# Kernel tuning notes

Measured on AMD Instinct MI355X. Metric: run time of the kernel, lower is better.

## Reference

```python
import jax, jax.numpy as jnp
import numpy as np
import math

D, H, HKV = 1024, 16, 4
DH = D // H  # 64
B, T = 2, 2048


def _rope_tables(T, Dh):
    pos = jnp.arange(T, dtype=jnp.float32)
    inv_freq = 1.0 / (10000.0 ** (jnp.arange(0, Dh, 2, dtype=jnp.float32) / Dh))
    ang = pos[:, None] * inv_freq[None, :]                 # [T, Dh/2]
    ang = jnp.concatenate([ang, ang], axis=-1)             # [T, Dh]
    return jnp.cos(ang)[None, None], jnp.sin(ang)[None, None]  # [1,1,T,Dh]


def setup_inputs() -> dict:
    key = jax.random.key(0)
    kx, kq, kk, kv, ko = jax.random.split(key, 5)
    x = jax.random.normal(kx, (B, T, D), dtype=jnp.float32)
    s = 1.0 / math.sqrt(D)
    Wq = jax.random.normal(kq, (H * DH, D), dtype=jnp.float32) * s
    Wk = jax.random.normal(kk, (HKV * DH, D), dtype=jnp.float32) * s
    Wv = jax.random.normal(kv, (HKV * DH, D), dtype=jnp.float32) * s
    Wo = jax.random.normal(ko, (D, D), dtype=jnp.float32) * s
    rope_cos, rope_sin = _rope_tables(T, DH)
    # additive causal mask: 0 on/below diagonal, -1e9 above
    causal = jnp.triu(jnp.full((T, T), -1e9, dtype=jnp.float32), k=1)[None, None]
    return {"x": x, "rope_cos": rope_cos, "rope_sin": rope_sin,
            "attn_mask": causal, "Wq": Wq, "Wk": Wk, "Wv": Wv, "Wo": Wo}


def _apply_rope(t, cos, sin):
    # t: [B,h,T,Dh]; cos/sin broadcast [1,1,T,Dh]
    Dh = t.shape[-1]
    t1, t2 = t[..., :Dh // 2], t[..., Dh // 2:]
    t_rot = jnp.concatenate([-t2, t1], axis=-1)
    Tlen = t.shape[2]
    return t * cos[..., :Tlen, :] + t_rot * sin[..., :Tlen, :]


def reference(x, rope_cos, rope_sin, attn_mask, Wq, Wk, Wv, Wo):
    Bx, Tx, Dx = x.shape
    q = (x @ Wq.T).reshape(Bx, Tx, H, DH).transpose(0, 2, 1, 3)    # [B,H,T,Dh]
    k = (x @ Wk.T).reshape(Bx, Tx, HKV, DH).transpose(0, 2, 1, 3)  # [B,Hkv,T,Dh]
    v = (x @ Wv.T).reshape(Bx, Tx, HKV, DH).transpose(0, 2, 1, 3)
    q = _apply_rope(q, rope_cos, rope_sin)
    k = _apply_rope(k, rope_cos, rope_sin)
    rep = H // HKV
    k = jnp.repeat(k, rep, axis=1)  # repeat_interleave on head dim
    v = jnp.repeat(v, rep, axis=1)
    att = jnp.einsum('bhtd,bhsd->bhts', q, k) / math.sqrt(DH)
    att = att + attn_mask
    att = jax.nn.softmax(att, axis=-1)
    y = jnp.einsum('bhts,bhsd->bhtd', att, v)
    y = y.transpose(0, 2, 1, 3).reshape(Bx, Tx, Dx)
    return y @ Wo.T
```

## Files before the change

### kernel.cpp

```cpp
#include <hip/hip_runtime.h>


typedef short bf16x8 __attribute__((ext_vector_type(8)));
typedef float f32x4 __attribute__((ext_vector_type(4)));

__device__ __forceinline__ unsigned short f2bf(float f) {
  unsigned u = __float_as_uint(f);
  u += 0x7fffu + ((u >> 16) & 1u);
  return (unsigned short)(u >> 16);
}

__device__ __forceinline__ unsigned cvt_pk_bf16(float lo, float hi) {
  unsigned r;
  asm("v_cvt_pk_bf16_f32 %0, %1, %2" : "=v"(r) : "v"(lo), "v"(hi));
  return r;
}

__device__ __forceinline__ float fexp2(float x) {
#if __has_builtin(__builtin_amdgcn_exp2f)
  return __builtin_amdgcn_exp2f(x);
#else
  return __expf(x * 0.69314718056f);
#endif
}

__device__ __forceinline__ void load_lds16(const void* g, void* l) {
  __builtin_amdgcn_global_load_lds(
      (const __attribute__((address_space(1))) void*)g,
      (__attribute__((address_space(3))) void*)l, 16, 0, 0);
}

__global__ __launch_bounds__(256) void cvt_all(const float* __restrict__ x,
                                               const float* __restrict__ Wq,
                                               const float* __restrict__ Wk,
                                               const float* __restrict__ Wv,
                                               const float* __restrict__ Wo,
                                               unsigned short* __restrict__ xb,
                                               unsigned short* __restrict__ Wcat,
                                               unsigned short* __restrict__ Wob) {
  int i = blockIdx.x * blockDim.x + threadIdx.x;
  const float* src; unsigned short* dst; int off;
  if (i < 1048576)      { src = x;  dst = xb;             off = i; }
  else if (i < 1310720) { src = Wq; dst = Wcat;           off = i - 1048576; }
  else if (i < 1376256) { src = Wk; dst = Wcat + 1048576; off = i - 1310720; }
  else if (i < 1441792) { src = Wv; dst = Wcat + 1310720; off = i - 1376256; }
  else                  { src = Wo; dst = Wob;            off = i - 1441792; }
  float4 v = reinterpret_cast<const float4*>(src)[off];
  ushort4 o;
  o.x = f2bf(v.x); o.y = f2bf(v.y); o.z = f2bf(v.z); o.w = f2bf(v.w);
  reinterpret_cast<ushort4*>(dst)[off] = o;
}

__global__ __launch_bounds__(256) void gemm_bt(const unsigned short* __restrict__ A,
                                               const unsigned short* __restrict__ B,
                                               float* __restrict__ C,
                                               int M, int N, int K) {
  __shared__ unsigned short As[2][128][32];
  __shared__ unsigned short Bs[2][64][32];
  const int tid  = threadIdx.x;
  const int lane = tid & 63, wave = tid >> 6;
  const int m0 = blockIdx.y * 128, n0 = blockIdx.x * 64;
  const int fr = lane & 15, k8 = (lane >> 4) * 8;
  const int nT = K >> 5;
  f32x4 acc[2][4] = {};
  const int ca0 = wave, ca1 = 4 + wave;
#define BT_STAGE(sel, kt)                                                        \
  {                                                                              \
    { const int c = ca0*64 + lane, row = c >> 2, col = (c & 3) * 8;              \
      load_lds16(A + (size_t)(m0 + row)*K + (kt) + col,                          \
                 (char*)&As[sel][0][0] + (size_t)ca0*1024); }                    \
    { const int c = ca1*64 + lane, row = c >> 2, col = (c & 3) * 8;              \
      load_lds16(A + (size_t)(m0 + row)*K + (kt) + col,                          \
                 (char*)&As[sel][0][0] + (size_t)ca1*1024); }                    \
    { const int c = ca0*64 + lane, row = c >> 2, col = (c & 3) * 8;              \
      load_lds16(B + (size_t)(n0 + row)*K + (kt) + col,                          \
                 (char*)&Bs[sel][0][0] + (size_t)ca0*1024); }                    \
  }
  BT_STAGE(0, 0);
  __syncthreads();
  for (int t = 0; t < nT; ++t) {
    const int cur = t & 1;
    if (t + 1 < nT) BT_STAGE(cur ^ 1, (t + 1) * 32);
    bf16x8 af[2], bf[4];
#pragma unroll
    for (int i = 0; i < 2; ++i) af[i] = *(const bf16x8*)&As[cur][wave*32 + i*16 + fr][k8];
#pragma unroll
    for (int i = 0; i < 4; ++i) bf[i] = *(const bf16x8*)&Bs[cur][i*16 + fr][k8];
#pragma unroll
    for (int mi = 0; mi < 2; ++mi)
#pragma unroll
      for (int ni = 0; ni < 4; ++ni)
        acc[mi][ni] = __builtin_amdgcn_mfma_f32_16x16x32_bf16(af[mi], bf[ni], acc[mi][ni], 0, 0, 0);
    __syncthreads();
  }
#pragma unroll
  for (int mi = 0; mi < 2; ++mi)
#pragma unroll
    for (int ni = 0; ni < 4; ++ni)
#pragma unroll
      for (int j = 0; j < 4; ++j) {
        int row = m0 + wave*32 + mi*16 + (lane >> 4)*4 + j;
        int col = n0 + ni*16 + fr;
        C[(size_t)row * N + col] = acc[mi][ni][j];
      }
}

__global__ __launch_bounds__(256) void gemm_qkv_rope(const unsigned short* __restrict__ A,
                                                     const unsigned short* __restrict__ Bw,
                                                     const float* __restrict__ rc,
                                                     const float* __restrict__ rs,
                                                     unsigned short* __restrict__ Qb,
                                                     unsigned short* __restrict__ Kb,
                                                     unsigned short* __restrict__ Vb) {
  const int K = 1024;
  __shared__ unsigned short As[2][128][32];
  __shared__ unsigned short Bs[2][64][32];
  const int tid  = threadIdx.x;
  const int lane = tid & 63, wave = tid >> 6;
  const int m0 = blockIdx.y * 128, n0 = blockIdx.x * 64;
  const int fr = lane & 15, k8 = (lane >> 4) * 8;
  f32x4 acc[2][4] = {};
  const int ca0 = wave, ca1 = 4 + wave;
#define QK_STAGE(sel, kt)                                                        \
  {                                                                              \
    { const int c = ca0*64 + lane, row = c >> 2, col = (c & 3) * 8;              \
      load_lds16(A + (size_t)(m0 + row)*K + (kt) + col,                          \
                 (char*)&As[sel][0][0] + (size_t)ca0*1024); }                    \
    { const int c = ca1*64 + lane, row = c >> 2, col = (c & 3) * 8;              \
      load_lds16(A + (size_t)(m0 + row)*K + (kt) + col,                          \
                 (char*)&As[sel][0][0] + (size_t)ca1*1024); }                    \
    { const int c = ca0*64 + lane, row = c >> 2, col = (c & 3) * 8;              \
      load_lds16(Bw + (size_t)(n0 + row)*K + (kt) + col,                         \
                 (char*)&Bs[sel][0][0] + (size_t)ca0*1024); }                    \
  }
  QK_STAGE(0, 0);
  __syncthreads();
  for (int t = 0; t < 32; ++t) {
    const int cur = t & 1;
    if (t + 1 < 32) QK_STAGE(cur ^ 1, (t + 1) * 32);
    bf16x8 af[2], bf[4];
#pragma unroll
    for (int i = 0; i < 2; ++i) af[i] = *(const bf16x8*)&As[cur][wave*32 + i*16 + fr][k8];
#pragma unroll
    for (int i = 0; i < 4; ++i) bf[i] = *(const bf16x8*)&Bs[cur][i*16 + fr][k8];
#pragma unroll
    for (int mi = 0; mi < 2; ++mi)
#pragma unroll
      for (int ni = 0; ni < 4; ++ni)
        acc[mi][ni] = __builtin_amdgcn_mfma_f32_16x16x32_bf16(af[mi], bf[ni], acc[mi][ni], 0, 0, 0);
    __syncthreads();
  }
  const int rg = lane >> 4;
  const float SCLQ = 0.125f * 1.44269504089f;
  const int colbase = n0;
#pragma unroll
  for (int mi = 0; mi < 2; ++mi) {
#pragma unroll
    for (int j = 0; j < 4; ++j) {
      const int m = m0 + wave*32 + mi*16 + rg*4 + j;
      const int b = m >> 11, t = m & 2047;
      if (colbase < 1280) {
        float vr[4];
#pragma unroll
        for (int ni = 0; ni < 4; ++ni) {
          const int d = ni*16 + fr;
          float cs = rc[t*64 + d], sn = rs[t*64 + d];
          float x = acc[mi][ni][j];
          float partner = acc[mi][ni ^ 2][j];
          float rot = (ni < 2) ? -partner : partner;
          vr[ni] = x * cs + rot * sn;
        }
        if (colbase < 1024) {
          const int h = colbase >> 6;
          size_t base = ((size_t)((b*16 + h)*2048 + t) << 6);
#pragma unroll
          for (int ni = 0; ni < 4; ++ni) Qb[base + ni*16 + fr] = f2bf(vr[ni] * SCLQ);
        } else {
          const int kh = (colbase - 1024) >> 6;
          size_t base = ((size_t)((b*4 + kh)*2048 + t) << 6);
#pragma unroll
          for (int ni = 0; ni < 4; ++ni) Kb[base + ni*16 + fr] = f2bf(vr[ni]);
        }
      } else {
        const int vh = (colbase - 1280) >> 6;
#pragma unroll
        for (int ni = 0; ni < 4; ++ni) {
          const int d = ni*16 + fr;
          Vb[((size_t)((b*4 + vh)*64 + d))*2048 + t] = f2bf(acc[mi][ni][j]);
        }
      }
    }
  }
}

__global__ __launch_bounds__(256) void attn_kernel(const unsigned short* __restrict__ Qb,
                                                   const unsigned short* __restrict__ Kb,
                                                   const unsigned short* __restrict__ Vb,
                                                   unsigned short* __restrict__ Yb) {
  __shared__ unsigned short Ks[2][64][72];
  __shared__ unsigned short Vt[2][64][72];
  __shared__ unsigned PpA[4][32][20];
  __shared__ unsigned PpB[4][32][20];
  const int p = blockIdx.x, bh = blockIdx.y;
  const int b = bh >> 4, h = bh & 15, kvh = h >> 2;
  const int qtA = 31 - p, qtB = p;
  const int nkv = qtA + 1;
  const int tid = threadIdx.x;
  const int wave = tid >> 6, lane = tid & 63;
  const int fr = lane & 15, g = lane >> 4, k8 = g * 8;
  const int srow = tid >> 3, scol = (tid & 7) * 8;
  const unsigned short* Kp = Kb + ((size_t)(b*4 + kvh)*2048) * 64;
  const unsigned short* Vp = Vb + ((size_t)(b*4 + kvh)*64) * 2048;
  const unsigned short* QpA = Qb + ((size_t)((b*16 + h)*2048 + qtA*64)) * 64;
  const unsigned short* QpB = Qb + ((size_t)((b*16 + h)*2048 + qtB*64)) * 64;
  bf16x8 qfA0 = *(const bf16x8*)(QpA + (wave*16 + fr)*64 + k8);
  bf16x8 qfA1 = *(const bf16x8*)(QpA + (wave*16 + fr)*64 + 32 + k8);
  bf16x8 qfB0 = *(const bf16x8*)(QpB + (wave*16 + fr)*64 + k8);
  bf16x8 qfB1 = *(const bf16x8*)(QpB + (wave*16 + fr)*64 + 32 + k8);
  float lsA = 0.f, lsB = 0.f;
  f32x4 accA[4] = {}, accB[4] = {};
  const int qgA = qtA*64 + wave*16 + fr;
  const int qgB = qtB*64 + wave*16 + fr;

  bf16x8 kreg[2], vreg[2];
#pragma unroll
  for (int j = 0; j < 2; ++j) {
    kreg[j] = *(const bf16x8*)(Kp + (size_t)(srow + j*32)*64 + scol);
    vreg[j] = *(const bf16x8*)(Vp + (size_t)(srow + j*32)*2048 + scol);
  }
#pragma unroll
  for (int j = 0; j < 2; ++j) {
    *(bf16x8*)&Ks[0][srow + j*32][scol] = kreg[j];
    *(bf16x8*)&Vt[0][srow + j*32][scol] = vreg[j];
  }
  __syncthreads();

  for (int kt = 0; kt < nkv; ++kt) {
    const int kv0 = kt * 64;
    const int cur = kt & 1;
    const bool actB = (kt <= qtB);
    const bool more = (kt + 1 < nkv);
    if (more) {
      const size_t nv0 = (size_t)(kt + 1) * 64;
#pragma unroll
      for (int j = 0; j < 2; ++j) {
        kreg[j] = *(const bf16x8*)(Kp + (nv0 + srow + j*32)*64 + scol);
        vreg[j] = *(const bf16x8*)(Vp + (size_t)(srow + j*32)*2048 + nv0 + scol);
      }
    }
    f32x4 sA[4] = {}, sB[4] = {};
    __builtin_amdgcn_s_setprio(1);
#pragma unroll
    for (int n = 0; n < 4; ++n) {
      bf16x8 kf0 = *(const bf16x8*)&Ks[cur][n*16 + fr][k8];
      sA[n] = __builtin_amdgcn_mfma_f32_16x16x32_bf16(kf0, qfA0, sA[n], 0, 0, 0);
      if (actB) sB[n] = __builtin_amdgcn_mfma_f32_16x16x32_bf16(kf0, qfB0, sB[n], 0, 0, 0);
      bf16x8 kf1 = *(const bf16x8*)&Ks[cur][n*16 + fr][32 + k8];
      sA[n] = __builtin_amdgcn_mfma_f32_16x16x32_bf16(kf1, qfA1, sA[n], 0, 0, 0);
      if (actB) sB[n] = __builtin_amdgcn_mfma_f32_16x16x32_bf16(kf1, qfB1, sB[n], 0, 0, 0);
    }
    __builtin_amdgcn_s_setprio(0);
    bf16x8 vf[2][4];
#pragma unroll
    for (int c = 0; c < 2; ++c)
#pragma unroll
      for (int dt = 0; dt < 4; ++dt)
        vf[c][dt] = *(const bf16x8*)&Vt[cur][dt*16 + fr][c*32 + k8];
    {
      const bool diag = (kt == qtA);
#pragma unroll
      for (int n = 0; n < 4; ++n)
#pragma unroll
        for (int r2 = 0; r2 < 2; ++r2) {
          float s0 = sA[n][2*r2], s1 = sA[n][2*r2 + 1];
          if (diag) {
            if (kv0 + n*16 + g*4 + 2*r2     > qgA) s0 = -3.0e38f;
            if (kv0 + n*16 + g*4 + 2*r2 + 1 > qgA) s1 = -3.0e38f;
          }
          float p0 = fexp2(s0);
          float p1 = fexp2(s1);
          lsA += p0 + p1;
          PpA[wave][n*8 + g*2 + r2][fr] = cvt_pk_bf16(p0, p1);
        }
    }
    if (actB) {
      const bool diag = (kt == qtB);
#pragma unroll
      for (int n = 0; n < 4; ++n)
#pragma unroll
        for (int r2 = 0; r2 < 2; ++r2) {
          float s0 = sB[n][2*r2], s1 = sB[n][2*r2 + 1];
          if (diag) {
            if (kv0 + n*16 + g*4 + 2*r2     > qgB) s0 = -3.0e38f;
            if (kv0 + n*16 + g*4 + 2*r2 + 1 > qgB) s1 = -3.0e38f;
          }
          float p0 = fexp2(s0);
          float p1 = fexp2(s1);
          lsB += p0 + p1;
          PpB[wave][n*8 + g*2 + r2][fr] = cvt_pk_bf16(p0, p1);
        }
    }
    __builtin_amdgcn_s_setprio(1);
#pragma unroll
    for (int c = 0; c < 2; ++c) {
      union { unsigned u[4]; bf16x8 v; } pa, pb;
#pragma unroll
      for (int i2 = 0; i2 < 4; ++i2) pa.u[i2] = PpA[wave][c*16 + g*4 + i2][fr];
      if (actB) {
#pragma unroll
        for (int i2 = 0; i2 < 4; ++i2) pb.u[i2] = PpB[wave][c*16 + g*4 + i2][fr];
      }
#pragma unroll
      for (int dt = 0; dt < 4; ++dt) {
        accA[dt] = __builtin_amdgcn_mfma_f32_16x16x32_bf16(vf[c][dt], pa.v, accA[dt], 0, 0, 0);
        if (actB) accB[dt] = __builtin_amdgcn_mfma_f32_16x16x32_bf16(vf[c][dt], pb.v, accB[dt], 0, 0, 0);
      }
    }
    __builtin_amdgcn_s_setprio(0);
    if (more) {
#pragma unroll
      for (int j = 0; j < 2; ++j) {
        *(bf16x8*)&Ks[cur ^ 1][srow + j*32][scol] = kreg[j];
        *(bf16x8*)&Vt[cur ^ 1][srow + j*32][scol] = vreg[j];
      }
      __syncthreads();
    }
  }
  {
    float ls = lsA;
    ls += __shfl_xor(ls, 16);
    ls += __shfl_xor(ls, 32);
    const float inv = 1.0f / ls;
    size_t base = ((size_t)(b*2048 + qgA) << 10) + h*64;
#pragma unroll
    for (int dt = 0; dt < 4; ++dt) {
      uint2 pk;
      pk.x = cvt_pk_bf16(accA[dt][0] * inv, accA[dt][1] * inv);
      pk.y = cvt_pk_bf16(accA[dt][2] * inv, accA[dt][3] * inv);
      *(uint2*)&Yb[base + dt*16 + g*4] = pk;
    }
  }
  {
    float ls = lsB;
    ls += __shfl_xor(ls, 16);
    ls += __shfl_xor(ls, 32);
    const float inv = 1.0f / ls;
    size_t base = ((size_t)(b*2048 + qgB) << 10) + h*64;
#pragma unroll
    for (int dt = 0; dt < 4; ++dt) {
      uint2 pk;
      pk.x = cvt_pk_bf16(accB[dt][0] * inv, accB[dt][1] * inv);
      pk.y = cvt_pk_bf16(accB[dt][2] * inv, accB[dt][3] * inv);
      *(uint2*)&Yb[base + dt*16 + g*4] = pk;
    }
  }
}

extern "C" void kernel_launch(void* const* d_in, const int* in_sizes, int n_in,
                              void* d_out, int out_size, void* d_ws, size_t ws_size,
                              hipStream_t stream) {
  const float* x  = (const float*)d_in[0];
  const float* rc = (const float*)d_in[1];
  const float* rs = (const float*)d_in[2];
  const float* Wq = (const float*)d_in[4];
  const float* Wk = (const float*)d_in[5];
  const float* Wv = (const float*)d_in[6];
  const float* Wo = (const float*)d_in[7];
  float* out = (float*)d_out;

  char* ws = (char*)d_ws;
  unsigned short* xb   = (unsigned short*)(ws);
  unsigned short* Wcat = (unsigned short*)(ws + 8388608);
  unsigned short* Wob  = (unsigned short*)(ws + 11534336);
  unsigned short* Qb   = (unsigned short*)(ws + 38797312);
  unsigned short* Kb   = (unsigned short*)(ws + 47185920);
  unsigned short* Vb   = (unsigned short*)(ws + 49283072);
  unsigned short* Yb   = (unsigned short*)(ws + 51380224);

  cvt_all<<<6656, 256, 0, stream>>>(x, Wq, Wk, Wv, Wo, xb, Wcat, Wob);
  gemm_qkv_rope<<<dim3(24, 32), 256, 0, stream>>>(xb, Wcat, rc, rs, Qb, Kb, Vb);
  attn_kernel<<<dim3(16, 32), 256, 0, stream>>>(Qb, Kb, Vb, Yb);
  gemm_bt<<<dim3(16, 32), 256, 0, stream>>>(Yb, Wob, out, 4096, 1024, 1024);
}
```

Baseline: 113.6 us.

## Split attention KV range across two blocks and add combine kernel

New measurement: 201.1 us. 1.77x slower.

```diff
diff --git a/kernel.cpp b/kernel.cpp
--- a/kernel.cpp
+++ b/kernel.cpp
@@ -22,6 +22,10 @@
 #else
   return __expf(x * 0.69314718056f);
 #endif
+}
+
+__device__ __forceinline__ float bf2f(unsigned short u) {
+  return __uint_as_float(((unsigned)u) << 16);
 }
 
 __device__ __forceinline__ void load_lds16(const void* g, void* l) {
@@ -193,15 +197,16 @@
   }
 }
 
-__global__ __launch_bounds__(256) void attn_kernel(const unsigned short* __restrict__ Qb,
-                                                   const unsigned short* __restrict__ Kb,
-                                                   const unsigned short* __restrict__ Vb,
-                                                   unsigned short* __restrict__ Yb) {
-  __shared__ unsigned short Ks[2][64][72];
-  __shared__ unsigned short Vt[2][64][72];
+__global__ __launch_bounds__(256, 4) void attn_kernel(const unsigned short* __restrict__ Qb,
+                                                      const unsigned short* __restrict__ Kb,
+                                                      const unsigned short* __restrict__ Vb,
+                                                      unsigned short* __restrict__ Po,
+                                                      float* __restrict__ Ls) {
+  __shared__ unsigned short Ks[64][72];
+  __shared__ unsigned short Vt[64][72];
   __shared__ unsigned PpA[4][32][20];
   __shared__ unsigned PpB[4][32][20];
-  const int p = blockIdx.x, bh = blockIdx.y;
+  const int p = blockIdx.x, bh = blockIdx.y, s = blockIdx.z;
   const int b = bh >> 4, h = bh & 15, kvh = h >> 2;
   const int qtA = 31 - p, qtB = p;
   const int nkv = qtA + 1;
@@ -225,37 +230,36 @@
   bf16x8 kreg[2], vreg[2];
 #pragma unroll
   for (int j = 0; j < 2; ++j) {
-    kreg[j] = *(const bf16x8*)(Kp + (size_t)(srow + j*32)*64 + scol);
-    vreg[j] = *(const bf16x8*)(Vp + (size_t)(srow + j*32)*2048 + scol);
-  }
-#pragma unroll
-  for (int j = 0; j < 2; ++j) {
-    *(bf16x8*)&Ks[0][srow + j*32][scol] = kreg[j];
-    *(bf16x8*)&Vt[0][srow + j*32][scol] = vreg[j];
-  }
-  __syncthreads();
-
-  for (int kt = 0; kt < nkv; ++kt) {
+    kreg[j] = *(const bf16x8*)(Kp + (size_t)(s*64 + srow + j*32)*64 + scol);
+    vreg[j] = *(const bf16x8*)(Vp + (size_t)(srow + j*32)*2048 + s*64 + scol);
+  }
+
+  for (int kt = s; kt < nkv; kt += 2) {
     const int kv0 = kt * 64;
-    const int cur = kt & 1;
     const bool actB = (kt <= qtB);
-    const bool more = (kt + 1 < nkv);
-    if (more) {
-      const size_t nv0 = (size_t)(kt + 1) * 64;
+    __syncthreads();
+#pragma unroll
+    for (int j = 0; j < 2; ++j) {
+      *(bf16x8*)&Ks[srow + j*32][scol] = kreg[j];
+      *(bf16x8*)&Vt[srow + j*32][scol] = vreg[j];
+    }
+    if (kt + 2 < nkv) {
+      const size_t nv0 = (size_t)(kt + 2) * 64;
 #pragma unroll
       for (int j = 0; j < 2; ++j) {
         kreg[j] = *(const bf16x8*)(Kp + (nv0 + srow + j*32)*64 + scol);
         vreg[j] = *(const bf16x8*)(Vp + (size_t)(srow + j*32)*2048 + nv0 + scol);
       }
     }
+    __syncthreads();
     f32x4 sA[4] = {}, sB[4] = {};
     __builtin_amdgcn_s_setprio(1);
 #pragma unroll
     for (int n = 0; n < 4; ++n) {
-      bf16x8 kf0 = *(const bf16x8*)&Ks[cur][n*16 + fr][k8];
+      bf16x8 kf0 = *(const bf16x8*)&Ks[n*16 + fr][k8];
       sA[n] = __builtin_amdgcn_mfma_f32_16x16x32_bf16(kf0, qfA0, sA[n], 0, 0, 0);
       if (actB) sB[n] = __builtin_amdgcn_mfma_f32_16x16x32_bf16(kf0, qfB0, sB[n], 0, 0, 0);
-      bf16x8 kf1 = *(const bf16x8*)&Ks[cur][n*16 + fr][32 + k8];
+      bf16x8 kf1 = *(const bf16x8*)&Ks[n*16 + fr][32 + k8];
       sA[n] = __builtin_amdgcn_mfma_f32_16x16x32_bf16(kf1, qfA1, sA[n], 0, 0, 0);
       if (actB) sB[n] = __builtin_amdgcn_mfma_f32_16x16x32_bf16(kf1, qfB1, sB[n], 0, 0, 0);
     }
@@ -265,7 +269,7 @@
     for (int c = 0; c < 2; ++c)
 #pragma unroll
       for (int dt = 0; dt < 4; ++dt)
-        vf[c][dt] = *(const bf16x8*)&Vt[cur][dt*16 + fr][c*32 + k8];
+        vf[c][dt] = *(const bf16x8*)&Vt[dt*16 + fr][c*32 + k8];
     {
       const bool diag = (kt == qtA);
 #pragma unroll
@@ -317,43 +321,58 @@
       }
     }
     __builtin_amdgcn_s_setprio(0);
-    if (more) {
-#pragma unroll
-      for (int j = 0; j < 2; ++j) {
-        *(bf16x8*)&Ks[cur ^ 1][srow + j*32][scol] = kreg[j];
-        *(bf16x8*)&Vt[cur ^ 1][srow + j*32][scol] = vreg[j];
-      }
-      __syncthreads();
-    }
   }
   {
     float ls = lsA;
     ls += __shfl_xor(ls, 16);
     ls += __shfl_xor(ls, 32);
-    const float inv = 1.0f / ls;
-    size_t base = ((size_t)(b*2048 + qgA) << 10) + h*64;
+    if (g == 0) Ls[((size_t)(s*32 + bh) << 11) + qgA] = ls;
+    size_t base = (((size_t)(s*32 + bh) << 11) + qgA) << 6;
 #pragma unroll
     for (int dt = 0; dt < 4; ++dt) {
       uint2 pk;
-      pk.x = cvt_pk_bf16(accA[dt][0] * inv, accA[dt][1] * inv);
-      pk.y = cvt_pk_bf16(accA[dt][2] * inv, accA[dt][3] * inv);
-      *(uint2*)&Yb[base + dt*16 + g*4] = pk;
+      pk.x = cvt_pk_bf16(accA[dt][0], accA[dt][1]);
+      pk.y = cvt_pk_bf16(accA[dt][2], accA[dt][3]);
+      *(uint2*)&Po[base + dt*16 + g*4] = pk;
     }
   }
   {
     float ls = lsB;
     ls += __shfl_xor(ls, 16);
     ls += __shfl_xor(ls, 32);
-    const float inv = 1.0f / ls;
-    size_t base = ((size_t)(b*2048 + qgB) << 10) + h*64;
+    if (g == 0) Ls[((size_t)(s*32 + bh) << 11) + qgB] = ls;
+    size_t base = (((size_t)(s*32 + bh) << 11) + qgB) << 6;
 #pragma unroll
     for (int dt = 0; dt < 4; ++dt) {
       uint2 pk;
-      pk.x = cvt_pk_bf16(accB[dt][0] * inv, accB[dt][1] * inv);
-      pk.y = cvt_pk_bf16(accB[dt][2] * inv, accB[dt][3] * inv);
-      *(uint2*)&Yb[base + dt*16 + g*4] = pk;
-    }
-  }
+      pk.x = cvt_pk_bf16(accB[dt][0], accB[dt][1]);
+      pk.y = cvt_pk_bf16(accB[dt][2], accB[dt][3]);
+      *(uint2*)&Po[base + dt*16 + g*4] = pk;
+    }
+  }
+}
+
+__global__ __launch_bounds__(256) void attn_combine(const unsigned short* __restrict__ Po,
+                                                    const float* __restrict__ Ls,
+                                                    unsigned short* __restrict__ Yb) {
+  int i = blockIdx.x * 256 + threadIdx.x;
+  int c8 = i & 7;
+  int t  = (i >> 3) & 2047;
+  int bh = i >> 14;
+  size_t o = (((size_t)(bh*2048 + t)) << 6) + c8*8;
+  uint4 a = *(const uint4*)(Po + o);
+  uint4 c = *(const uint4*)(Po + 4194304 + o);
+  float inv = 1.0f / (Ls[bh*2048 + t] + Ls[65536 + bh*2048 + t]);
+  unsigned ra[4], au[4] = {a.x, a.y, a.z, a.w}, cu[4] = {c.x, c.y, c.z, c.w};
+#pragma unroll
+  for (int w = 0; w < 4; ++w) {
+    float lo = (bf2f((unsigned short)(au[w] & 0xffff)) + bf2f((unsigned short)(cu[w] & 0xffff))) * inv;
+    float hi = (bf2f((unsigned short)(au[w] >> 16))    + bf2f((unsigned short)(cu[w] >> 16)))    * inv;
+    ra[w] = cvt_pk_bf16(lo, hi);
+  }
+  int b_ = bh >> 4, h = bh & 15;
+  uint4 r; r.x = ra[0]; r.y = ra[1]; r.z = ra[2]; r.w = ra[3];
+  *(uint4*)&Yb[(((size_t)(b_*2048 + t)) << 10) + h*64 + c8*8] = r;
 }
 
 extern "C" void kernel_launch(void* const* d_in, const int* in_sizes, int n_in,
@@ -372,6 +391,8 @@
   unsigned short* xb   = (unsigned short*)(ws);
   unsigned short* Wcat = (unsigned short*)(ws + 8388608);
   unsigned short* Wob  = (unsigned short*)(ws + 11534336);
+  unsigned short* Po   = (unsigned short*)(ws + 13631488);
+  float*          Ls   = (float*)(ws + 30408704);
   unsigned short* Qb   = (unsigned short*)(ws + 38797312);
   unsigned short* Kb   = (unsigned short*)(ws + 47185920);
   unsigned short* Vb   = (unsigned short*)(ws + 49283072);
@@ -379,6 +400,7 @@
 
   cvt_all<<<6656, 256, 0, stream>>>(x, Wq, Wk, Wv, Wo, xb, Wcat, Wob);
   gemm_qkv_rope<<<dim3(24, 32), 256, 0, stream>>>(xb, Wcat, rc, rs, Qb, Kb, Vb);
-  attn_kernel<<<dim3(16, 32), 256, 0, stream>>>(Qb, Kb, Vb, Yb);
+  attn_kernel<<<dim3(16, 32, 2), 256, 0, stream>>>(Qb, Kb, Vb, Po, Ls);
+  attn_combine<<<2048, 256, 0, stream>>>(Po, Ls, Yb);
   gemm_bt<<<dim3(16, 32), 256, 0, stream>>>(Yb, Wob, out, 4096, 1024, 1024);
 }
```
